# Optimization experiments

Hardware: AMD Instinct MI355X
Metric: run time of the kernel (lower is better)

## Reference

```python
import jax, jax.numpy as jnp
import numpy as np

N_NODES = 100000
N_EDGES = 1600000
D_IN = 128
D_HID = 128
N_CLS = 40


def setup_inputs() -> dict:
    key = jax.random.key(0)
    ks = jax.random.split(key, 8)
    x = jax.random.normal(ks[0], (N_NODES, D_IN), dtype=jnp.float32)
    edge_index = jax.random.randint(ks[1], (2, N_EDGES), 0, N_NODES, dtype=jnp.int64)
    s = 1.0 / np.sqrt(D_IN)
    W1_l = jax.random.normal(ks[2], (D_IN, D_HID), dtype=jnp.float32) * s
    W1_r = jax.random.normal(ks[3], (D_IN, D_HID), dtype=jnp.float32) * s
    b1 = jnp.zeros((D_HID,), dtype=jnp.float32)
    s2 = 1.0 / np.sqrt(D_HID)
    W2_l = jax.random.normal(ks[4], (D_HID, N_CLS), dtype=jnp.float32) * s2
    W2_r = jax.random.normal(ks[5], (D_HID, N_CLS), dtype=jnp.float32) * s2
    b2 = jnp.zeros((N_CLS,), dtype=jnp.float32)
    return {"x": x, "edge_index": edge_index, "W1_l": W1_l, "W1_r": W1_r,
            "b1": b1, "W2_l": W2_l, "W2_r": W2_r, "b2": b2}


def _sage_conv(x, src, dst, Wl, Wr, b):
    # mean-aggregate neighbor features (PyG SAGEConv, aggr='mean')
    n = x.shape[0]
    agg = jax.ops.segment_sum(x[src], dst, num_segments=n)           # [N, d]
    deg = jax.ops.segment_sum(jnp.ones_like(dst, dtype=x.dtype), dst, num_segments=n)
    mean = agg / jnp.maximum(deg, 1.0)[:, None]
    # lin_l(mean) + bias + lin_r(x_root)  (lin_r has no bias in PyG)
    return mean @ Wl + b + x @ Wr


def reference(x, edge_index, W1_l, W1_r, b1, W2_l, W2_r, b2):
    src, dst = edge_index[0], edge_index[1]
    h = jax.nn.relu(_sage_conv(x, src, dst, W1_l, W1_r, b1))
    # F.dropout(training=...) is identity in eval mode (deterministic reference)
    out = _sage_conv(h, src, dst, W2_l, W2_r, b2)
    return jax.nn.softmax(out, axis=1)
```

## Files before the change

kernel.cpp:

```cpp
#include <hip/hip_runtime.h>

#define DIM 128
#define NCLS 40
#define NBIN 256
#define BINSH 9
#define CHUNK 4096

typedef unsigned short ushort_t;
typedef __attribute__((ext_vector_type(8))) short bf16x8;
typedef __attribute__((ext_vector_type(4))) float f32x4;

__device__ __forceinline__ ushort_t f2b(float f) {
    union { float f; unsigned u; } v; v.f = f;
    unsigned r = v.u + 0x7FFFu + ((v.u >> 16) & 1u);
    return (ushort_t)(r >> 16);
}

__device__ __forceinline__ float b2f(ushort_t b) {
    union { unsigned u; float f; } v; v.u = ((unsigned)b) << 16;
    return v.f;
}

__device__ __forceinline__ void acc_fp8x4(float4& a, int w) {
    a.x += __builtin_amdgcn_cvt_f32_fp8(w, 0);
    a.y += __builtin_amdgcn_cvt_f32_fp8(w, 1);
    a.z += __builtin_amdgcn_cvt_f32_fp8(w, 2);
    a.w += __builtin_amdgcn_cvt_f32_fp8(w, 3);
}

__global__ __launch_bounds__(256) void prep_kernel(
    const float* __restrict__ x, ushort_t* __restrict__ xbf, unsigned* __restrict__ xq,
    const float* __restrict__ W1r, const float* __restrict__ W1l, ushort_t* __restrict__ Wp,
    const float* __restrict__ W2l, ushort_t* __restrict__ Wp2,
    int* __restrict__ binCnt, int n4, int cb)
{
    const int b = blockIdx.x;
    if (b < cb) {
        int i = b * 256 + threadIdx.x;
        if (i >= n4) return;
        f32x4 v = __builtin_nontemporal_load(((const f32x4*)x) + i);
        ushort4 o;
        o.x = f2b(v.x); o.y = f2b(v.y); o.z = f2b(v.z); o.w = f2b(v.w);
        ((ushort4*)xbf)[i] = o;
        int p = __builtin_amdgcn_cvt_pk_fp8_f32(v.x, v.y, 0, false);
        p = __builtin_amdgcn_cvt_pk_fp8_f32(v.z, v.w, p, true);
        xq[i] = (unsigned)p;
    } else if (b < cb + 128) {
        int o = (b - cb) * 256 + threadIdx.x;
        int j    = o & 7;
        int lane = (o >> 3) & 63;
        int t    = (o >> 9) & 7;
        int kc   = o >> 12;
        int k = kc * 32 + (lane >> 4) * 8 + j;
        int nn = t * 16 + (lane & 15);
        float v = (k < DIM) ? W1r[k * DIM + nn] : W1l[(k - DIM) * DIM + nn];
        Wp[o] = f2b(v);
    } else if (b < cb + 152) {
        int o = (b - cb - 128) * 256 + threadIdx.x;
        int j    = o & 7;
        int lane = (o >> 3) & 63;
        int rem  = o >> 9;
        int t    = rem % 3;
        int kc   = rem / 3;
        int k  = kc * 32 + (lane >> 4) * 8 + j;
        int nn = t * 16 + (lane & 15);
        Wp2[o] = (nn < NCLS) ? f2b(W2l[k * NCLS + nn]) : (ushort_t)0;
    } else {
        binCnt[threadIdx.x] = 0;
    }
}


__global__ __launch_bounds__(256) void bincount_kernel(const int* __restrict__ dst,
                                                       int* __restrict__ binCnt, int E) {
    __shared__ int hist[NBIN];
    hist[threadIdx.x] = 0;
    __syncthreads();
    const int tid = blockIdx.x * 256 + threadIdx.x;
    const int stride = gridDim.x * 256;
    for (int e = tid; e < E; e += stride)
        atomicAdd(&hist[__builtin_nontemporal_load(dst + e) >> BINSH], 1);
    __syncthreads();
    if (hist[threadIdx.x]) atomicAdd(&binCnt[threadIdx.x], hist[threadIdx.x]);
}

__global__ __launch_bounds__(NBIN) void binscan_kernel(const int* __restrict__ binCnt,
                                                       int* __restrict__ binBase,
                                                       int* __restrict__ binCtr,
                                                       int* __restrict__ row_ptr, int n) {
    __shared__ int sc[NBIN];
    const int t = threadIdx.x;
    sc[t] = binCnt[t];
    __syncthreads();
    for (int off = 1; off < NBIN; off <<= 1) {
        int v = (t >= off) ? sc[t - off] : 0;
        __syncthreads();
        sc[t] += v;
        __syncthreads();
    }
    int excl = (t == 0) ? 0 : sc[t - 1];
    binBase[t] = excl;
    binCtr[t]  = excl;
    if (t == NBIN - 1) { binBase[NBIN] = sc[t]; row_ptr[n] = sc[t]; }
}

__global__ __launch_bounds__(256) void binscatter_kernel(
    const int* __restrict__ src, const int* __restrict__ dst,
    int* __restrict__ binCtr, int2* __restrict__ pairs, int E)
{
    __shared__ int ss[CHUNK];
    __shared__ int sd[CHUNK];
    __shared__ int hist[NBIN];
    __shared__ int base[NBIN];
    __shared__ int cnt[NBIN];
    const int nchunk = (E + CHUNK - 1) / CHUNK;
    for (int c = blockIdx.x; c < nchunk; c += gridDim.x) {
        const int e0 = c * CHUNK;
        const int m = min(CHUNK, E - e0);
        for (int i = threadIdx.x; i < m; i += 256) {
            ss[i] = __builtin_nontemporal_load(src + e0 + i);
            sd[i] = __builtin_nontemporal_load(dst + e0 + i);
        }
        hist[threadIdx.x] = 0;
        cnt[threadIdx.x] = 0;
        __syncthreads();
        for (int i = threadIdx.x; i < m; i += 256)
            atomicAdd(&hist[sd[i] >> BINSH], 1);
        __syncthreads();
        base[threadIdx.x] = hist[threadIdx.x]
            ? atomicAdd(&binCtr[threadIdx.x], hist[threadIdx.x]) : 0;
        __syncthreads();
        for (int i = threadIdx.x; i < m; i += 256) {
            int d = sd[i];
            int b = d >> BINSH;
            int off = base[b] + atomicAdd(&cnt[b], 1);
            pairs[off] = make_int2(ss[i], d);
        }
        __syncthreads();
    }
}

__global__ __launch_bounds__(256) void bincsr_kernel(
    const int2* __restrict__ pairs, const int* __restrict__ binBase,
    int* __restrict__ row_ptr, int* __restrict__ eidx, int n)
{
    __shared__ int deg[512];
    __shared__ int sc[512];
    __shared__ int cnt[512];
    const int b  = blockIdx.x;
    const int lo = binBase[b];
    const int hi = binBase[b + 1];
    const int nlo = b << BINSH;
    const int t = threadIdx.x;
    deg[t] = 0; deg[t + 256] = 0;
    cnt[t] = 0; cnt[t + 256] = 0;
    __syncthreads();
    for (int e = lo + t; e < hi; e += 256) {
        int2 p = pairs[e];
        atomicAdd(&deg[p.y - nlo], 1);
    }
    __syncthreads();
    sc[t] = deg[t];
    sc[t + 256] = deg[t + 256];
    __syncthreads();
    for (int off = 1; off < 512; off <<= 1) {
        int v0 = (t >= off) ? sc[t - off] : 0;
        int v1 = sc[t + 256 - off];
        __syncthreads();
        sc[t] += v0;
        sc[t + 256] += v1;
        __syncthreads();
    }
    {
        int node0 = nlo + t;
        int node1 = nlo + t + 256;
        if (node0 < n) row_ptr[node0] = lo + sc[t] - deg[t];
        if (node1 < n) row_ptr[node1] = lo + sc[t + 256] - deg[t + 256];
    }
    for (int e = lo + t; e < hi; e += 256) {
        int2 p = pairs[e];
        int dl = p.y - nlo;
        int slot = sc[dl] - deg[dl] + atomicAdd(&cnt[dl], 1);
        eidx[lo + slot] = p.x;
    }
}


__global__ __launch_bounds__(256) void gather128_kernel(
    const unsigned* __restrict__ xq, const int* __restrict__ row_ptr,
    const int* __restrict__ eidx, ushort_t* __restrict__ Bbf, int n)
{
    int t = blockIdx.x * 256 + threadIdx.x;
    int node = t >> 5;
    if (node >= n) return;
    int q = t & 31;
    int j  = row_ptr[node];
    int je = row_ptr[node + 1];
    const float id = 1.0f / fmaxf((float)(je - j), 1.0f);
    float4 acc = make_float4(0.f, 0.f, 0.f, 0.f);
    for (; j + 3 < je; j += 4) {
        int s0 = eidx[j], s1 = eidx[j + 1], s2 = eidx[j + 2], s3 = eidx[j + 3];
        int w0 = (int)xq[(size_t)s0 * 32 + q];
        int w1 = (int)xq[(size_t)s1 * 32 + q];
        int w2 = (int)xq[(size_t)s2 * 32 + q];
        int w3 = (int)xq[(size_t)s3 * 32 + q];
        acc_fp8x4(acc, w0); acc_fp8x4(acc, w1);
        acc_fp8x4(acc, w2); acc_fp8x4(acc, w3);
    }
    for (; j < je; ++j) {
        int s0 = eidx[j];
        acc_fp8x4(acc, (int)xq[(size_t)s0 * 32 + q]);
    }
    ushort4 o;
    o.x = f2b(acc.x * id); o.y = f2b(acc.y * id);
    o.z = f2b(acc.z * id); o.w = f2b(acc.w * id);
    ((ushort4*)(Bbf + (size_t)node * DIM))[q] = o;
}

__global__ __launch_bounds__(256) void mfma_gemm_kernel(
    const ushort_t* __restrict__ xbf, const ushort_t* __restrict__ mxbf,
    const ushort_t* __restrict__ Wp, const ushort_t* __restrict__ Wp2,
    const float* __restrict__ bias,
    ushort_t* __restrict__ Hbf, ushort_t* __restrict__ Cbf, int n)
{
    __shared__ ushort_t hl[4][16 * 136];
    const int wave = threadIdx.x >> 6;
    const int lane = threadIdx.x & 63;
    const int m16  = lane & 15;
    const int quad = lane >> 4;
    const int row0 = blockIdx.x * 64 + wave * 16;
    int arow = row0 + m16;
    if (arow >= n) arow = n - 1;
    f32x4 acc[8];
    #pragma unroll
    for (int t = 0; t < 8; ++t) acc[t] = (f32x4){0.f, 0.f, 0.f, 0.f};
    const ushort_t* __restrict__ xrow = xbf  + (size_t)arow * DIM;
    const ushort_t* __restrict__ mrow = mxbf + (size_t)arow * DIM;
    #pragma unroll
    for (int kc = 0; kc < 8; ++kc) {
        const int kcol = (kc & 3) * 32 + quad * 8;
        const bf16x8 afrag = *(const bf16x8*)((kc < 4 ? xrow : mrow) + kcol);
        const ushort_t* __restrict__ wp = Wp + (size_t)kc * 4096 + (size_t)lane * 8;
        #pragma unroll
        for (int t = 0; t < 8; ++t) {
            const bf16x8 bfrag = *(const bf16x8*)(wp + (size_t)t * 512);
            acc[t] = __builtin_amdgcn_mfma_f32_16x16x32_bf16(afrag, bfrag, acc[t], 0, 0, 0);
        }
    }
    ushort_t* __restrict__ hw = hl[wave];
    #pragma unroll
    for (int t = 0; t < 8; ++t) {
        const int col = t * 16 + m16;
        const float bv = bias[col];
        #pragma unroll
        for (int r = 0; r < 4; ++r) {
            hw[(quad * 4 + r) * 136 + col] = f2b(fmaxf(acc[t][r] + bv, 0.f));
        }
    }
    f32x4 acc2[3];
    #pragma unroll
    for (int t = 0; t < 3; ++t) acc2[t] = (f32x4){0.f, 0.f, 0.f, 0.f};
    const bool rowok = (row0 + m16) < n;
    #pragma unroll
    for (int kc = 0; kc < 4; ++kc) {
        const bf16x8 afrag2 = *(const bf16x8*)(hw + m16 * 136 + kc * 32 + quad * 8);
        if (rowok)
            *(bf16x8*)(Hbf + (size_t)(row0 + m16) * DIM + kc * 32 + quad * 8) = afrag2;
        const ushort_t* __restrict__ wp2 = Wp2 + (size_t)kc * 1536 + (size_t)lane * 8;
        #pragma unroll
        for (int t = 0; t < 3; ++t) {
            const bf16x8 bfrag = *(const bf16x8*)(wp2 + (size_t)t * 512);
            acc2[t] = __builtin_amdgcn_mfma_f32_16x16x32_bf16(afrag2, bfrag, acc2[t], 0, 0, 0);
        }
    }
    #pragma unroll
    for (int t = 0; t < 3; ++t) {
        const int col = t * 16 + m16;
        if (col >= NCLS) continue;
        #pragma unroll
        for (int r = 0; r < 4; ++r) {
            const int row = row0 + quad * 4 + r;
            if (row < n) Cbf[(size_t)row * NCLS + col] = f2b(acc2[t][r]);
        }
    }
}

__global__ __launch_bounds__(256) void final_kernel(
    const ushort_t* __restrict__ Hbf, const ushort_t* __restrict__ Cbf,
    const int* __restrict__ row_ptr, const int* __restrict__ eidx,
    const float* __restrict__ W, const float* __restrict__ b2,
    float* __restrict__ out, int n)
{
    int nd = blockIdx.x * 256 + threadIdx.x;
    if (nd >= n) return;
    int j  = row_ptr[nd];
    int je = row_ptr[nd + 1];
    const float id = 1.0f / fmaxf((float)(je - j), 1.0f);
    float lg[NCLS];
    #pragma unroll
    for (int c = 0; c < NCLS; ++c) lg[c] = 0.f;
    for (; j < je; ++j) {
        int s = eidx[j];
        const bf16x8* __restrict__ crow = (const bf16x8*)(Cbf + (size_t)s * NCLS);
        #pragma unroll
        for (int kk = 0; kk < 5; ++kk) {
            bf16x8 v = crow[kk];
            #pragma unroll
            for (int e = 0; e < 8; ++e)
                lg[kk * 8 + e] += b2f((ushort_t)v[e]);
        }
    }
    #pragma unroll
    for (int c = 0; c < NCLS; ++c) lg[c] = fmaf(lg[c], id, b2[c]);
    const ushort_t* __restrict__ h = Hbf + (size_t)nd * DIM;
    for (int k = 0; k < DIM; k += 4) {
        const ushort4 hu = *(const ushort4*)(h + k);
        const float hx = b2f(hu.x), hy = b2f(hu.y), hz = b2f(hu.z), hw = b2f(hu.w);
        const float* __restrict__ w0 = W + (size_t)(k + 0) * NCLS;
        const float* __restrict__ w1 = W + (size_t)(k + 1) * NCLS;
        const float* __restrict__ w2 = W + (size_t)(k + 2) * NCLS;
        const float* __restrict__ w3 = W + (size_t)(k + 3) * NCLS;
        #pragma unroll
        for (int c = 0; c < NCLS; ++c) {
            float acc = lg[c];
            acc = fmaf(hx, w0[c], acc);
            acc = fmaf(hy, w1[c], acc);
            acc = fmaf(hz, w2[c], acc);
            acc = fmaf(hw, w3[c], acc);
            lg[c] = acc;
        }
    }
    float m = lg[0];
    #pragma unroll
    for (int c = 1; c < NCLS; ++c) m = fmaxf(m, lg[c]);
    float s = 0.f;
    #pragma unroll
    for (int c = 0; c < NCLS; ++c) { lg[c] = __expf(lg[c] - m); s += lg[c]; }
    const float inv = 1.0f / s;
    float* __restrict__ o = out + (size_t)nd * NCLS;
    #pragma unroll
    for (int c = 0; c < NCLS; ++c) o[c] = lg[c] * inv;
}

extern "C" void kernel_launch(void* const* d_in, const int* in_sizes, int n_in,
                              void* d_out, int out_size, void* d_ws, size_t ws_size,
                              hipStream_t stream) {
    const float* x   = (const float*)d_in[0];
    const int*   ei  = (const int*)d_in[1];
    const float* W1l = (const float*)d_in[2];
    const float* W1r = (const float*)d_in[3];
    const float* b1  = (const float*)d_in[4];
    const float* W2l = (const float*)d_in[5];
    const float* W2r = (const float*)d_in[6];
    const float* b2  = (const float*)d_in[7];
    float* out = (float*)d_out;

    const int n = in_sizes[0] / DIM;
    const int E = in_sizes[1] / 2;
    const int* src = ei;
    const int* dst = ei + E;

    ushort_t* xbf     = (ushort_t*)d_ws;
    ushort_t* mxbf    = xbf + (size_t)n * DIM;
    ushort_t* Hbf     = mxbf + (size_t)n * DIM;
    ushort_t* Cbf     = Hbf + (size_t)n * DIM;
    unsigned* xq      = (unsigned*)(Cbf + (size_t)n * NCLS);
    ushort_t* Wp      = (ushort_t*)(xq + (size_t)n * 32);
    ushort_t* Wp2     = Wp + 256 * DIM;
    int*      eidx    = (int*)(Wp2 + 4 * 1536);
    int2*     pairs   = (int2*)(eidx + E);
    int*      row_ptr = (int*)(pairs + E);
    int*      binCnt  = row_ptr + (n + 1);
    int*      binBase = binCnt + NBIN;
    int*      binCtr  = binBase + NBIN + 1;

    const int n4 = n * 32;
    const int cb = (n4 + 255) / 256;
    prep_kernel<<<cb + 153, 256, 0, stream>>>(x, xbf, xq, W1r, W1l, Wp,
                                              W2l, Wp2, binCnt, n4, cb);

    bincount_kernel  <<<512, 256, 0, stream>>>(dst, binCnt, E);
    binscan_kernel   <<<1, NBIN, 0, stream>>>(binCnt, binBase, binCtr, row_ptr, n);
    binscatter_kernel<<<512, 256, 0, stream>>>(src, dst, binCtr, pairs, E);
    bincsr_kernel    <<<NBIN, 256, 0, stream>>>(pairs, binBase, row_ptr, eidx, n);

    {
        long long t = (long long)n * 32;
        gather128_kernel<<<(int)((t + 255) / 256), 256, 0, stream>>>(xq, row_ptr, eidx, mxbf, n);
    }
    mfma_gemm_kernel<<<(n + 63) / 64, 256, 0, stream>>>(xbf, mxbf, Wp, Wp2, b1, Hbf, Cbf, n);

    final_kernel<<<(n + 255) / 256, 256, 0, stream>>>(Hbf, Cbf, row_ptr, eidx, W2r, b2, out, n);
}
```

Before: 318.7 us.

## Split final kernel classes across four waves per node block

The final kernel now gives each node four threads (one per wavefront), each owning 10 of the 40 classes. Each thread gathers its slice of neighbor rows with 4-way unrolled loads and does its share of the root GEMV. Partial logits are then combined through shared memory for a single-wave softmax. This targets the register pressure and low occupancy of the 40-float per-thread accumulator and adds memory-level parallelism, at the cost of a block sync and an idle softmax phase in three of four waves.

```diff
diff --git a/kernel.cpp b/kernel.cpp
--- a/kernel.cpp
+++ b/kernel.cpp
@@ -9,6 +9,7 @@
 typedef unsigned short ushort_t;
 typedef __attribute__((ext_vector_type(8))) short bf16x8;
 typedef __attribute__((ext_vector_type(4))) float f32x4;
+typedef unsigned int uint4_u __attribute__((ext_vector_type(4), aligned(4)));
 
 __device__ __forceinline__ ushort_t f2b(float f) {
     union { float f; unsigned u; } v; v.f = f;
@@ -26,6 +27,22 @@
     a.y += __builtin_amdgcn_cvt_f32_fp8(w, 1);
     a.z += __builtin_amdgcn_cvt_f32_fp8(w, 2);
     a.w += __builtin_amdgcn_cvt_f32_fp8(w, 3);
+}
+
+__device__ __forceinline__ void acc_pair(float& a, float& b, unsigned u) {
+    union { unsigned x; float f; } lo, hi;
+    lo.x = u << 16;
+    hi.x = u & 0xFFFF0000u;
+    a += lo.f;
+    b += hi.f;
+}
+
+__device__ __forceinline__ void accv10(float* lg, uint4_u v, unsigned w) {
+    acc_pair(lg[0], lg[1], v.x);
+    acc_pair(lg[2], lg[3], v.y);
+    acc_pair(lg[4], lg[5], v.z);
+    acc_pair(lg[6], lg[7], v.w);
+    acc_pair(lg[8], lg[9], w);
 }
 
 __global__ __launch_bounds__(256) void prep_kernel(
@@ -291,55 +308,75 @@
     const float* __restrict__ W, const float* __restrict__ b2,
     float* __restrict__ out, int n)
 {
-    int nd = blockIdx.x * 256 + threadIdx.x;
-    if (nd >= n) return;
-    int j  = row_ptr[nd];
-    int je = row_ptr[nd + 1];
-    const float id = 1.0f / fmaxf((float)(je - j), 1.0f);
-    float lg[NCLS];
-    #pragma unroll
-    for (int c = 0; c < NCLS; ++c) lg[c] = 0.f;
-    for (; j < je; ++j) {
-        int s = eidx[j];
-        const bf16x8* __restrict__ crow = (const bf16x8*)(Cbf + (size_t)s * NCLS);
-        #pragma unroll
-        for (int kk = 0; kk < 5; ++kk) {
-            bf16x8 v = crow[kk];
+    __shared__ float lgs[64][41];
+    const int q    = threadIdx.x >> 6;
+    const int lane = threadIdx.x & 63;
+    const int node = blockIdx.x * 64 + lane;
+    const int c0   = q * 10;
+    float lg[10];
+    #pragma unroll
+    for (int c = 0; c < 10; ++c) lg[c] = 0.f;
+    if (node < n) {
+        int j  = row_ptr[node];
+        int je = row_ptr[node + 1];
+        const float id = 1.0f / fmaxf((float)(je - j), 1.0f);
+        for (; j + 3 < je; j += 4) {
+            int s0 = eidx[j], s1 = eidx[j + 1], s2 = eidx[j + 2], s3 = eidx[j + 3];
+            const ushort_t* p0 = Cbf + (size_t)s0 * NCLS + c0;
+            const ushort_t* p1 = Cbf + (size_t)s1 * NCLS + c0;
+            const ushort_t* p2 = Cbf + (size_t)s2 * NCLS + c0;
+            const ushort_t* p3 = Cbf + (size_t)s3 * NCLS + c0;
+            uint4_u a0 = *(const uint4_u*)p0; unsigned e0 = *(const unsigned*)(p0 + 8);
+            uint4_u a1 = *(const uint4_u*)p1; unsigned e1 = *(const unsigned*)(p1 + 8);
+            uint4_u a2 = *(const uint4_u*)p2; unsigned e2 = *(const unsigned*)(p2 + 8);
+            uint4_u a3 = *(const uint4_u*)p3; unsigned e3 = *(const unsigned*)(p3 + 8);
+            accv10(lg, a0, e0); accv10(lg, a1, e1);
+            accv10(lg, a2, e2); accv10(lg, a3, e3);
+        }
+        for (; j < je; ++j) {
+            const ushort_t* p0 = Cbf + (size_t)eidx[j] * NCLS + c0;
+            uint4_u a0 = *(const uint4_u*)p0; unsigned e0 = *(const unsigned*)(p0 + 8);
+            accv10(lg, a0, e0);
+        }
+        #pragma unroll
+        for (int c = 0; c < 10; ++c) lg[c] = fmaf(lg[c], id, b2[c0 + c]);
+        const ushort_t* __restrict__ h = Hbf + (size_t)node * DIM;
+        for (int k = 0; k < DIM; k += 4) {
+            const ushort4 hu = *(const ushort4*)(h + k);
+            const float hx = b2f(hu.x), hy = b2f(hu.y), hz = b2f(hu.z), hw = b2f(hu.w);
+            const float* __restrict__ w0 = W + (size_t)(k + 0) * NCLS + c0;
+            const float* __restrict__ w1 = W + (size_t)(k + 1) * NCLS + c0;
+            const float* __restrict__ w2 = W + (size_t)(k + 2) * NCLS + c0;
+            const float* __restrict__ w3 = W + (size_t)(k + 3) * NCLS + c0;
             #pragma unroll
-            for (int e = 0; e < 8; ++e)
-                lg[kk * 8 + e] += b2f((ushort_t)v[e]);
-        }
-    }
-    #pragma unroll
-    for (int c = 0; c < NCLS; ++c) lg[c] = fmaf(lg[c], id, b2[c]);
-    const ushort_t* __restrict__ h = Hbf + (size_t)nd * DIM;
-    for (int k = 0; k < DIM; k += 4) {
-        const ushort4 hu = *(const ushort4*)(h + k);
-        const float hx = b2f(hu.x), hy = b2f(hu.y), hz = b2f(hu.z), hw = b2f(hu.w);
-        const float* __restrict__ w0 = W + (size_t)(k + 0) * NCLS;
-        const float* __restrict__ w1 = W + (size_t)(k + 1) * NCLS;
-        const float* __restrict__ w2 = W + (size_t)(k + 2) * NCLS;
-        const float* __restrict__ w3 = W + (size_t)(k + 3) * NCLS;
-        #pragma unroll
-        for (int c = 0; c < NCLS; ++c) {
-            float acc = lg[c];
-            acc = fmaf(hx, w0[c], acc);
-            acc = fmaf(hy, w1[c], acc);
-            acc = fmaf(hz, w2[c], acc);
-            acc = fmaf(hw, w3[c], acc);
-            lg[c] = acc;
-        }
-    }
-    float m = lg[0];
-    #pragma unroll
-    for (int c = 1; c < NCLS; ++c) m = fmaxf(m, lg[c]);
-    float s = 0.f;
-    #pragma unroll
-    for (int c = 0; c < NCLS; ++c) { lg[c] = __expf(lg[c] - m); s += lg[c]; }
-    const float inv = 1.0f / s;
-    float* __restrict__ o = out + (size_t)nd * NCLS;
-    #pragma unroll
-    for (int c = 0; c < NCLS; ++c) o[c] = lg[c] * inv;
+            for (int c = 0; c < 10; ++c) {
+                float a = lg[c];
+                a = fmaf(hx, w0[c], a);
+                a = fmaf(hy, w1[c], a);
+                a = fmaf(hz, w2[c], a);
+                a = fmaf(hw, w3[c], a);
+                lg[c] = a;
+            }
+        }
+    }
+    #pragma unroll
+    for (int c = 0; c < 10; ++c) lgs[lane][c0 + c] = lg[c];
+    __syncthreads();
+    if (q == 0 && node < n) {
+        float v[NCLS];
+        #pragma unroll
+        for (int c = 0; c < NCLS; ++c) v[c] = lgs[lane][c];
+        float m = v[0];
+        #pragma unroll
+        for (int c = 1; c < NCLS; ++c) m = fmaxf(m, v[c]);
+        float s = 0.f;
+        #pragma unroll
+        for (int c = 0; c < NCLS; ++c) { v[c] = __expf(v[c] - m); s += v[c]; }
+        const float inv = 1.0f / s;
+        float* __restrict__ o = out + (size_t)node * NCLS;
+        #pragma unroll
+        for (int c = 0; c < NCLS; ++c) o[c] = v[c] * inv;
+    }
 }
 
 extern "C" void kernel_launch(void* const* d_in, const int* in_sizes, int n_in,
@@ -390,5 +427,5 @@
     }
     mfma_gemm_kernel<<<(n + 63) / 64, 256, 0, stream>>>(xbf, mxbf, Wp, Wp2, b1, Hbf, Cbf, n);
 
-    final_kernel<<<(n + 255) / 256, 256, 0, stream>>>(Hbf, Cbf, row_ptr, eidx, W2r, b2, out, n);
-}
+    final_kernel<<<(n + 63) / 64, 256, 0, stream>>>(Hbf, Cbf, row_ptr, eidx, W2r, b2, out, n);
+}
```

New measurement: 400.4 us. 1.26x slower.
